# Performance work log

Hardware: AMD Instinct MI355X
Metric: run time of the kernel (lower is better)

## Reference

```python
import jax, jax.numpy as jnp
import numpy as np

MIN_N = 4
MAX_N = 5
MIN_FREQ = 2 ** MIN_N  # 16
DT = 0.005
W = 1.0e6
HUBER = 0.005
N0 = 5
EPS_VAR = 1e-6


def _skew(v):
    x, y, z = v[..., 0], v[..., 1], v[..., 2]
    o = jnp.zeros_like(x)
    return jnp.stack([
        jnp.stack([o, -z, y], -1),
        jnp.stack([z, o, -x], -1),
        jnp.stack([-y, x, o], -1)], -2)


def so3_exp(phi):
    """Rodrigues formula: axis-angle (M,3) -> rotation matrices (M,3,3)."""
    a2 = jnp.sum(phi * phi, axis=-1)
    small = a2 < 1e-12
    a2s = jnp.where(small, 1.0, a2)
    a = jnp.sqrt(a2s)
    sin_t = jnp.where(small, 1.0 - a2 / 6.0, jnp.sin(a) / a)
    cos_t = jnp.where(small, 0.5 - a2 / 24.0, (1.0 - jnp.cos(a)) / a2s)
    Wm = _skew(phi)
    I = jnp.eye(3, dtype=phi.dtype)
    return I + sin_t[..., None, None] * Wm + cos_t[..., None, None] * jnp.matmul(Wm, Wm)


def so3_log(R):
    """Rotation matrices (M,3,3) -> axis-angle (M,3)."""
    tr = R[..., 0, 0] + R[..., 1, 1] + R[..., 2, 2]
    cos = jnp.clip(0.5 * (tr - 1.0), -1.0 + 1e-6, 1.0 - 1e-6)
    angle = jnp.arccos(cos)
    small = angle < 1e-6
    factor = jnp.where(small, 0.5, angle / (2.0 * jnp.sin(jnp.where(small, 1.0, angle))))
    # vee(R - R^T)
    w = jnp.stack([R[..., 2, 1] - R[..., 1, 2],
                   R[..., 0, 2] - R[..., 2, 0],
                   R[..., 1, 0] - R[..., 0, 1]], -1)
    return factor[..., None] * w


def _smooth_l1_mean(x):
    ax = jnp.abs(x)
    return jnp.mean(jnp.where(ax < 1.0, 0.5 * ax * ax, ax - 0.5))


def _f_huber(rs):
    return W * _smooth_l1_mean(rs / HUBER) * HUBER ** 2


def _pairwise(R):
    # drot[::2] @ drot[1::2]
    return jnp.matmul(R[::2], R[1::2])


def _bmtm_log(A, B):
    # SO3.log(A^T B)
    return so3_log(jnp.einsum('nij,nik->njk', A, B))


def setup_inputs() -> dict:
    key = jax.random.key(0)
    ks = jax.random.split(key, 5)
    N, T = 128, 16384
    return {
        'w_hat': jax.random.normal(ks[0], (N, T, 3), jnp.float32),
        'dw_16': jax.random.normal(ks[1], (N, T, 3), jnp.float32),
        'w_gt': jax.random.normal(ks[2], (N, T, 3), jnp.float32),
        'w_mean': jax.random.normal(ks[3], (N, T, 3), jnp.float32),
        'w_std': jax.random.uniform(ks[4], (N, T, 3), jnp.float32),
    }


def reference(w_hat, dw_16, w_gt, w_mean, w_std):
    N = dw_16.shape[0]
    # --- gyro loss ---
    drot_16 = so3_exp(dw_16[:, ::MIN_FREQ].reshape(-1, 3))
    drot_hat = so3_exp(DT * w_hat.reshape(-1, 3))
    for _ in range(MIN_N):
        drot_hat = _pairwise(drot_hat)
    rs = _bmtm_log(drot_hat, drot_16).reshape(N, -1, 3)[:, N0:]
    gyro16 = _f_huber(rs)
    gyro32 = jnp.zeros((), rs.dtype)
    for k in range(MIN_N, MAX_N):
        drot_hat = _pairwise(drot_hat)
        drot_16 = _pairwise(drot_16)
        rs = _bmtm_log(drot_hat, drot_16).reshape(N, -1, 3)[:, N0:]
        gyro32 = _f_huber(rs) / 2 ** (k - MIN_N + 1) / 2.0
    # --- gaussian NLL ---
    w_var = w_std ** 2
    w_var = jnp.where(w_var < EPS_VAR, EPS_VAR, w_var)
    gap = w_gt - w_hat
    gnll = jnp.mean((jnp.log(w_var) + (gap - w_mean) ** 2 / w_var) / 2.0)
    return gyro16 + gyro32 + gnll
```

## Files before the change

kernel.cpp:

```cpp
#include <hip/hip_runtime.h>

#define THREADS 256
#define NQUAD 524288
#define BLOCKS (NQUAD / THREADS)
#define DT 0.005f
#define INV_HUBER 200.0f

#define NELEM 6291456.0
#define CNT16 391296.0
#define CNT32 194688.0

__device__ __forceinline__ float rcpf(float x) {
    return __builtin_amdgcn_rcpf(x);
}

__device__ __forceinline__ float acos_poly(float x) {
    float ax = fabsf(x);
    float p = fmaf(ax, -0.0012624911f, 0.0066700901f);
    p = fmaf(ax, p, -0.0170881256f);
    p = fmaf(ax, p, 0.0308918810f);
    p = fmaf(ax, p, -0.0501743046f);
    p = fmaf(ax, p, 0.0889789874f);
    p = fmaf(ax, p, -0.2145988016f);
    p = fmaf(ax, p, 1.5707963050f);
    float r = sqrtf(fmaxf(1.0f - ax, 0.0f)) * p;
    return x < 0.0f ? 3.14159265358979f - r : r;
}

__device__ __forceinline__ void so3_exp_small(float x, float y, float z, float R[9]) {
    float a2 = x * x + y * y + z * z;
    float st = 1.0f - a2 * (1.0f / 6.0f) * (1.0f - a2 * (1.0f / 20.0f));
    float ct = 0.5f - a2 * (1.0f / 24.0f) * (1.0f - a2 * (1.0f / 30.0f));
    R[0] = 1.0f + ct * (x * x - a2);
    R[1] = ct * (x * y) - st * z;
    R[2] = ct * (x * z) + st * y;
    R[3] = ct * (x * y) + st * z;
    R[4] = 1.0f + ct * (y * y - a2);
    R[5] = ct * (y * z) - st * x;
    R[6] = ct * (x * z) - st * y;
    R[7] = ct * (y * z) + st * x;
    R[8] = 1.0f + ct * (z * z - a2);
}

__device__ __forceinline__ void so3_exp_full(float x, float y, float z, float R[9]) {
    float a2 = x * x + y * y + z * z;
    bool sm = a2 < 1e-12f;
    float a2s = sm ? 1.0f : a2;
    float a = sqrtf(a2s);
    float s = __sinf(a);
    float c = __cosf(a);
    float st = sm ? (1.0f - a2 * (1.0f / 6.0f)) : (s * rcpf(a));
    float ct = sm ? (0.5f - a2 * (1.0f / 24.0f)) : ((1.0f - c) * rcpf(a2s));
    R[0] = 1.0f + ct * (x * x - a2);
    R[1] = ct * (x * y) - st * z;
    R[2] = ct * (x * z) + st * y;
    R[3] = ct * (x * y) + st * z;
    R[4] = 1.0f + ct * (y * y - a2);
    R[5] = ct * (y * z) - st * x;
    R[6] = ct * (x * z) - st * y;
    R[7] = ct * (y * z) + st * x;
    R[8] = 1.0f + ct * (z * z - a2);
}

__device__ __forceinline__ void mm3(const float A[9], const float B[9], float C[9]) {
#pragma unroll
    for (int i = 0; i < 3; ++i) {
        float a0 = A[3 * i], a1 = A[3 * i + 1], a2 = A[3 * i + 2];
        C[3 * i + 0] = a0 * B[0] + a1 * B[3] + a2 * B[6];
        C[3 * i + 1] = a0 * B[1] + a1 * B[4] + a2 * B[7];
        C[3 * i + 2] = a0 * B[2] + a1 * B[5] + a2 * B[8];
    }
}

__device__ __forceinline__ float huber_bmtm(const float A[9], const float B[9]) {
    float tr = 0.f, w0 = 0.f, w1 = 0.f, w2 = 0.f;
#pragma unroll
    for (int k = 0; k < 3; ++k) {
        float a0 = A[3 * k], a1 = A[3 * k + 1], a2v = A[3 * k + 2];
        float b0 = B[3 * k], b1 = B[3 * k + 1], b2v = B[3 * k + 2];
        tr += a0 * b0 + a1 * b1 + a2v * b2v;
        w0 += a2v * b1 - a1 * b2v;
        w1 += a0 * b2v - a2v * b0;
        w2 += a1 * b0 - a0 * b1;
    }
    float cs = 0.5f * (tr - 1.0f);
    cs = fminf(fmaxf(cs, -1.0f + 1e-6f), 1.0f - 1e-6f);
    float ang = acos_poly(cs);
    float sn = sqrtf(fmaxf(1.0f - cs * cs, 0.0f));
    float fac = ang * 0.5f * rcpf(sn);
    float h = 0.0f, r;
    r = fabsf(fac * w0 * INV_HUBER); h += (r < 1.0f) ? 0.5f * r * r : (r - 0.5f);
    r = fabsf(fac * w1 * INV_HUBER); h += (r < 1.0f) ? 0.5f * r * r : (r - 0.5f);
    r = fabsf(fac * w2 * INV_HUBER); h += (r < 1.0f) ? 0.5f * r * r : (r - 0.5f);
    return h;
}

__device__ __forceinline__ float gnll4(float4 h, float4 g, float4 m, float4 s) {
    float p = 0.f;
#pragma unroll
    for (int k = 0; k < 4; ++k) {
        float hv = (&h.x)[k], gv = (&g.x)[k], mv = (&m.x)[k], sv = (&s.x)[k];
        float v = fmaxf(sv * sv, 1e-6f);
        float d = gv - hv - mv;
        float rv = rcpf(v);
        rv = rv * (2.0f - v * rv);
        p += __logf(v) + d * d * rv;
    }
    return p;
}

__global__ __launch_bounds__(THREADS) void dg_loss_kernel(
    const float* __restrict__ w_hat, const float* __restrict__ dw16,
    const float* __restrict__ w_gt, const float* __restrict__ w_mean,
    const float* __restrict__ w_std, double* __restrict__ partial)
{
    const int tid = threadIdx.x;
    const int t = blockIdx.x * THREADS + tid;
    const int lane = tid & 63;

    __shared__ float4 swh[768];

    const size_t base = (size_t)blockIdx.x * 768;
    const float4* h4 = (const float4*)w_hat;
    const float4* g4 = (const float4*)w_gt;
    const float4* m4 = (const float4*)w_mean;
    const float4* s4 = (const float4*)w_std;
    float4 H[3], G[3], M[3], S[3];
#pragma unroll
    for (int k = 0; k < 3; ++k) {
        H[k] = h4[base + k * 256 + tid];
        G[k] = g4[base + k * 256 + tid];
        M[k] = m4[base + k * 256 + tid];
        S[k] = s4[base + k * 256 + tid];
    }
    const int b = t >> 2;
    float4 q4 = ((const float4*)dw16)[(size_t)b * 12];

#pragma unroll
    for (int k = 0; k < 3; ++k)
        swh[k * 256 + tid] = H[k];
    __syncthreads();

    double lg = 0.5 * (double)(gnll4(H[0], G[0], M[0], S[0]) +
                               gnll4(H[1], G[1], M[1], S[1]) +
                               gnll4(H[2], G[2], M[2], S[2]));

    float4 r0 = swh[tid * 3 + 0];
    float4 r1 = swh[tid * 3 + 1];
    float4 r2 = swh[tid * 3 + 2];

    float E0[9], E1[9], E2[9], E3[9], T01[9], T23[9], P[9];
    so3_exp_small(DT * r0.x, DT * r0.y, DT * r0.z, E0);
    so3_exp_small(DT * r0.w, DT * r1.x, DT * r1.y, E1);
    so3_exp_small(DT * r1.z, DT * r1.w, DT * r2.x, E2);
    so3_exp_small(DT * r2.y, DT * r2.z, DT * r2.w, E3);
    mm3(E0, E1, T01);
    mm3(E2, E3, T23);
    mm3(T01, T23, P);

#pragma unroll
    for (int s = 1; s <= 2; s <<= 1) {
        float Nb[9];
#pragma unroll
        for (int e = 0; e < 9; ++e) Nb[e] = __shfl_xor(P[e], s);
        const bool rt = (lane & s) != 0;
        float A[9], B[9], T[9];
#pragma unroll
        for (int e = 0; e < 9; ++e) { A[e] = rt ? Nb[e] : P[e]; B[e] = rt ? P[e] : Nb[e]; }
        mm3(A, B, T);
#pragma unroll
        for (int e = 0; e < 9; ++e) P[e] = T[e];
    }

    float Q[9];
    so3_exp_full(q4.x, q4.y, q4.z, Q);

    float Pn[9], Qn[9];
#pragma unroll
    for (int e = 0; e < 9; ++e) {
        Pn[e] = __shfl_xor(P[e], 4);
        Qn[e] = __shfl_xor(Q[e], 4);
    }
    float T1[9], T2[9];
    mm3(P, Pn, T1);
    mm3(Q, Qn, T2);
    const bool role16 = (lane & 3) == 0;
    const bool role32 = (lane & 7) == 1;
    float A[9], B[9];
#pragma unroll
    for (int e = 0; e < 9; ++e) {
        A[e] = role16 ? P[e] : T1[e];
        B[e] = role16 ? Q[e] : T2[e];
    }
    float hub = huber_bmtm(A, B);
    double lh16 = 0.0, lh32 = 0.0;
    if (role16 && ((b & 1023) >= 5)) lh16 = (double)hub;
    const int c = t >> 3;
    if (role32 && ((c & 511) >= 5)) lh32 = (double)hub;

    double part = lg * (1.0 / NELEM) + lh16 * (25.0 / CNT16) + lh32 * (6.25 / CNT32);
    __shared__ double s_p[4];
#pragma unroll
    for (int off = 32; off > 0; off >>= 1)
        part += __shfl_down(part, off);
    const int wv = tid >> 6;
    if (lane == 0) s_p[wv] = part;
    __syncthreads();
    if (tid == 0)
        partial[blockIdx.x] = s_p[0] + s_p[1] + s_p[2] + s_p[3];
}

__global__ __launch_bounds__(THREADS) void finalize_kernel(
    const double* __restrict__ partial, float* __restrict__ out)
{
    double s = 0.0;
#pragma unroll
    for (int i = 0; i < BLOCKS / THREADS; ++i)
        s += partial[i * THREADS + threadIdx.x];
    __shared__ double s_p[4];
#pragma unroll
    for (int off = 32; off > 0; off >>= 1)
        s += __shfl_down(s, off);
    const int lane = threadIdx.x & 63, wv = threadIdx.x >> 6;
    if (lane == 0) s_p[wv] = s;
    __syncthreads();
    if (threadIdx.x == 0)
        out[0] = (float)(s_p[0] + s_p[1] + s_p[2] + s_p[3]);
}

extern "C" void kernel_launch(void* const* d_in, const int* in_sizes, int n_in,
                              void* d_out, int out_size, void* d_ws, size_t ws_size,
                              hipStream_t stream) {
    const float* w_hat = (const float*)d_in[0];
    const float* dw16 = (const float*)d_in[1];
    const float* w_gt = (const float*)d_in[2];
    const float* w_mean = (const float*)d_in[3];
    const float* w_std = (const float*)d_in[4];
    float* out = (float*)d_out;
    double* partial = (double*)d_ws;

    dg_loss_kernel<<<BLOCKS, THREADS, 0, stream>>>(
        w_hat, dw16, w_gt, w_mean, w_std, partial);
    finalize_kernel<<<1, THREADS, 0, stream>>>(partial, out);
}
```

Measured before the change: 147.5 us.

## Assign two timesteps per thread and extend shuffle tree to eight lanes

Each thread now handles two samples instead of four. It loads float2 triples directly and drops the shared-memory staging and block barrier. The pairwise rotation reduction adds one more xor-shuffle level, and the 16/32 roles are remapped to match. This doubles the thread count and block count to expose more parallelism and cut per-thread registers. In exchange it adds more shuffles, redundant matrix products in idle lanes, float2 loads that are strided across threads, and twice as many partial sums for finalize to read.

```diff
diff --git a/kernel.cpp b/kernel.cpp
--- a/kernel.cpp
+++ b/kernel.cpp
@@ -1,8 +1,8 @@
 #include <hip/hip_runtime.h>
 
 #define THREADS 256
-#define NQUAD 524288
-#define BLOCKS (NQUAD / THREADS)
+#define NPAIR 1048576
+#define BLOCKS (NPAIR / THREADS)
 #define DT 0.005f
 #define INV_HUBER 200.0f
 
@@ -95,10 +95,10 @@
     return h;
 }
 
-__device__ __forceinline__ float gnll4(float4 h, float4 g, float4 m, float4 s) {
+__device__ __forceinline__ float gnll2(float2 h, float2 g, float2 m, float2 s) {
     float p = 0.f;
 #pragma unroll
-    for (int k = 0; k < 4; ++k) {
+    for (int k = 0; k < 2; ++k) {
         float hv = (&h.x)[k], gv = (&g.x)[k], mv = (&m.x)[k], sv = (&s.x)[k];
         float v = fmaxf(sv * sv, 1e-6f);
         float d = gv - hv - mv;
@@ -118,48 +118,29 @@
     const int t = blockIdx.x * THREADS + tid;
     const int lane = tid & 63;
 
-    __shared__ float4 swh[768];
-
-    const size_t base = (size_t)blockIdx.x * 768;
-    const float4* h4 = (const float4*)w_hat;
-    const float4* g4 = (const float4*)w_gt;
-    const float4* m4 = (const float4*)w_mean;
-    const float4* s4 = (const float4*)w_std;
-    float4 H[3], G[3], M[3], S[3];
-#pragma unroll
-    for (int k = 0; k < 3; ++k) {
-        H[k] = h4[base + k * 256 + tid];
-        G[k] = g4[base + k * 256 + tid];
-        M[k] = m4[base + k * 256 + tid];
-        S[k] = s4[base + k * 256 + tid];
-    }
-    const int b = t >> 2;
+    const float2* h2 = (const float2*)w_hat;
+    const float2* g2 = (const float2*)w_gt;
+    const float2* m2 = (const float2*)w_mean;
+    const float2* s2 = (const float2*)w_std;
+    const size_t p3 = (size_t)t * 3;
+    float2 Ha = h2[p3], Hb = h2[p3 + 1], Hc = h2[p3 + 2];
+    float2 Ga = g2[p3], Gb = g2[p3 + 1], Gc = g2[p3 + 2];
+    float2 Ma = m2[p3], Mb = m2[p3 + 1], Mc = m2[p3 + 2];
+    float2 Sa = s2[p3], Sb = s2[p3 + 1], Sc = s2[p3 + 2];
+    const int b = t >> 3;
     float4 q4 = ((const float4*)dw16)[(size_t)b * 12];
 
-#pragma unroll
-    for (int k = 0; k < 3; ++k)
-        swh[k * 256 + tid] = H[k];
-    __syncthreads();
-
-    double lg = 0.5 * (double)(gnll4(H[0], G[0], M[0], S[0]) +
-                               gnll4(H[1], G[1], M[1], S[1]) +
-                               gnll4(H[2], G[2], M[2], S[2]));
-
-    float4 r0 = swh[tid * 3 + 0];
-    float4 r1 = swh[tid * 3 + 1];
-    float4 r2 = swh[tid * 3 + 2];
-
-    float E0[9], E1[9], E2[9], E3[9], T01[9], T23[9], P[9];
-    so3_exp_small(DT * r0.x, DT * r0.y, DT * r0.z, E0);
-    so3_exp_small(DT * r0.w, DT * r1.x, DT * r1.y, E1);
-    so3_exp_small(DT * r1.z, DT * r1.w, DT * r2.x, E2);
-    so3_exp_small(DT * r2.y, DT * r2.z, DT * r2.w, E3);
-    mm3(E0, E1, T01);
-    mm3(E2, E3, T23);
-    mm3(T01, T23, P);
-
-#pragma unroll
-    for (int s = 1; s <= 2; s <<= 1) {
+    double lg = 0.5 * (double)(gnll2(Ha, Ga, Ma, Sa) +
+                               gnll2(Hb, Gb, Mb, Sb) +
+                               gnll2(Hc, Gc, Mc, Sc));
+
+    float E0[9], E1[9], P[9];
+    so3_exp_small(DT * Ha.x, DT * Ha.y, DT * Hb.x, E0);
+    so3_exp_small(DT * Hb.y, DT * Hc.x, DT * Hc.y, E1);
+    mm3(E0, E1, P);
+
+#pragma unroll
+    for (int s = 1; s <= 4; s <<= 1) {
         float Nb[9];
 #pragma unroll
         for (int e = 0; e < 9; ++e) Nb[e] = __shfl_xor(P[e], s);
@@ -178,14 +159,14 @@
     float Pn[9], Qn[9];
 #pragma unroll
     for (int e = 0; e < 9; ++e) {
-        Pn[e] = __shfl_xor(P[e], 4);
-        Qn[e] = __shfl_xor(Q[e], 4);
+        Pn[e] = __shfl_xor(P[e], 8);
+        Qn[e] = __shfl_xor(Q[e], 8);
     }
     float T1[9], T2[9];
     mm3(P, Pn, T1);
     mm3(Q, Qn, T2);
-    const bool role16 = (lane & 3) == 0;
-    const bool role32 = (lane & 7) == 1;
+    const bool role16 = (lane & 7) == 0;
+    const bool role32 = (lane & 15) == 1;
     float A[9], B[9];
 #pragma unroll
     for (int e = 0; e < 9; ++e) {
@@ -195,7 +176,7 @@
     float hub = huber_bmtm(A, B);
     double lh16 = 0.0, lh32 = 0.0;
     if (role16 && ((b & 1023) >= 5)) lh16 = (double)hub;
-    const int c = t >> 3;
+    const int c = t >> 4;
     if (role32 && ((c & 511) >= 5)) lh32 = (double)hub;
 
     double part = lg * (1.0 / NELEM) + lh16 * (25.0 / CNT16) + lh32 * (6.25 / CNT32);
```

After: 147.7 us. About the same (+0.2%).
